# Performance work log

Hardware: AMD Instinct MI355X
Metric: run time of the kernel (lower is better)

## Reference

```python
import jax, jax.numpy as jnp
import numpy as np

B, T, F, H, K = 512, 128, 256, 512, 3

def setup_inputs() -> dict:
    key = jax.random.key(0)
    ks = jax.random.split(key, 8)
    x = jax.random.normal(ks[0], (B, T, F), dtype=jnp.float32)
    theta = jnp.ones((F,), dtype=jnp.float32)                 # selector logits
    Wx = jax.random.normal(ks[1], (F, H), dtype=jnp.float32) * 0.1
    Wh = jax.random.normal(ks[2], (H, H), dtype=jnp.float32) * 0.1
    b = jnp.zeros((H,), dtype=jnp.float32)
    c = jax.random.normal(ks[3], (H, K), dtype=jnp.float32)   # fuzzy centers
    sigma = jnp.ones((H, K), dtype=jnp.float32)               # fuzzy widths
    q = jax.random.normal(ks[4], (H, K), dtype=jnp.float32)   # rule consequents
    Wc = jax.random.normal(ks[5], (H, 1), dtype=jnp.float32) * 0.05  # classifier
    bc = jnp.zeros((1,), dtype=jnp.float32)
    return dict(x=x, theta=theta, Wx=Wx, Wh=Wh, b=b, c=c, sigma=sigma, q=q, Wc=Wc, bc=bc)


def reference(x, theta, Wx, Wh, b, c, sigma, q, Wc, bc):
    weights = jax.nn.sigmoid(theta)                 # [F]
    xf = x * weights                                # [B,T,F]
    # x_t @ Wx is used twice per step (for z_t and new_info); precompute once for all t.
    xw = jnp.einsum('btf,fh->bth', xf, Wx)          # [B,T,H]
    new_info = jnp.tanh(xw)                         # [B,T,H]
    inv_den = 1.0 / (2.0 * sigma ** 2 + 1e-8)       # [H,K]

    def step(h, inp):
        xw_t, new_t = inp                           # [B,H], [B,H]
        z = xw_t + h @ Wh + b                       # [B,H]
        mu = jnp.exp(-(z[..., None] - c) ** 2 * inv_den)   # [B,H,K]
        g = jax.nn.sigmoid(jnp.sum(mu * q, axis=-1) / (jnp.sum(mu, axis=-1) + 1e-8))
        h = (1.0 - g) * h + g * new_t
        return h, None

    h0 = jnp.zeros((x.shape[0], Wh.shape[0]), dtype=x.dtype)
    h, _ = jax.lax.scan(step, h0, (jnp.swapaxes(xw, 0, 1), jnp.swapaxes(new_info, 0, 1)))
    logits = h @ Wc + bc                            # [B,1]
    return logits, weights
```

## Files before the change

kernel.cpp:

```cpp
#include <hip/hip_runtime.h>
#include <hip/hip_bf16.h>


#define B_  512
#define T_  128
#define F_  256
#define H_  512
#define LOG2E 1.4426950408889634f

#define XW_T_STRIDE 262144

typedef __attribute__((ext_vector_type(8))) short short8;
typedef __attribute__((ext_vector_type(4))) float float4v;
typedef __attribute__((ext_vector_type(4))) int int4i;

__device__ inline ushort f2bf(float f) {
  __hip_bfloat16 h = __float2bfloat16(f);
  return *reinterpret_cast<ushort*>(&h);
}
__device__ inline float bf2f(unsigned u) { return __uint_as_float(u << 16); }
__device__ inline float fexp2(float x) { return __builtin_amdgcn_exp2f(x); }
__device__ inline float frcp(float x) { return __builtin_amdgcn_rcpf(x); }

#define WS_W2I8 67108864
#define WS_WXF  67371008
#define WS_GP8  67633152
#define WS_BVEC 67649536
#define WS_WCV  67651584
#define WS_SCOL 67653632
#define WS_WTS  67657728

__global__ __launch_bounds__(256) void prep_weights(
    const float* __restrict__ Wh, const float* __restrict__ Wx,
    const float* __restrict__ theta, const float* __restrict__ b,
    const float* __restrict__ c, const float* __restrict__ sigma,
    const float* __restrict__ q, const float* __restrict__ Wc,
    int* __restrict__ W2, ushort* __restrict__ WxF,
    float* __restrict__ scol, float* __restrict__ out_w,
    float* __restrict__ gp8, float* __restrict__ bvec,
    float* __restrict__ wcv, float* __restrict__ wts) {
  __shared__ float lds[16544];
  const int t = threadIdx.x;

  if (blockIdx.x < 32) {
    const int nb = blockIdx.x;
    const int cc = t & 15, rg = t >> 4;
    float m = 0.f;
#pragma unroll
    for (int s = 0; s < 32; ++s)
      m = fmaxf(m, fabsf(Wh[(rg + s * 16) * H_ + nb * 16 + cc]));
    lds[rg * 16 + cc] = m;
    __syncthreads();
    if (t < 16) {
      float mm = lds[t];
#pragma unroll
      for (int s = 1; s < 16; ++s) mm = fmaxf(mm, lds[s * 16 + t]);
      mm = fmaxf(mm, 1e-20f);
      scol[nb * 16 + t] = mm / (127.f * 127.f);
      lds[256 + t] = 127.f / mm;
    }
    __syncthreads();
    const int lane = t & 63, dw = t >> 6;
    const int n = nb * 16 + (lane & 15);
    const float iv = lds[256 + (lane & 15)];
#pragma unroll
    for (int kt = 0; kt < 8; ++kt) {
      int pk = 0;
#pragma unroll
      for (int jj = 0; jj < 4; ++jj) {
        const int k = kt * 64 + ((lane >> 4) << 4) + dw * 4 + jj;
        int qv = (int)rintf(Wh[k * H_ + n] * iv);
        qv = min(127, max(-127, qv));
        pk |= (qv & 255) << (8 * jj);
      }
      W2[((kt * 32 + nb) * 64 + lane) * 4 + dw] = pk;
    }
  } else if (blockIdx.x < 40) {
    const int kt = blockIdx.x - 32;
#pragma unroll
    for (int it = 0; it < 16; ++it) {
      const int lin = (it * 256 + t) * 4;
      const float4 v = *(const float4*)(Wx + kt * 32 * H_ + lin);
      const int f = lin >> 9, n0 = lin & 511;
      lds[f * 517 + n0 + 0] = v.x;
      lds[f * 517 + n0 + 1] = v.y;
      lds[f * 517 + n0 + 2] = v.z;
      lds[f * 517 + n0 + 3] = v.w;
    }
    __syncthreads();
#pragma unroll
    for (int it = 0; it < 8; ++it) {
      const int o = (it * 256 + t) * 8;
      const int lane = (o >> 3) & 63, nb = o >> 9;
      const int n = nb * 16 + (lane & 15), fb = (lane >> 4) << 3;
      ushort v[8];
#pragma unroll
      for (int j = 0; j < 8; ++j) v[j] = f2bf(lds[(fb + j) * 517 + n]);
      *(short8*)(WxF + kt * 16384 + o) = *(short8*)v;
    }
  } else {
#pragma unroll
    for (int r = 0; r < 2; ++r) {
      const int i = t + r * 256;
      if (i < F_) {
        float w = 1.f / (1.f + __expf(-theta[i]));
        out_w[i] = w;
        wts[i] = w;
      }
      float a[3], cc[3], qq[3];
#pragma unroll
      for (int k = 0; k < 3; ++k) {
        float s = sigma[i * 3 + k];
        cc[k] = c[i * 3 + k];
        a[k] = -LOG2E / (2.f * s * s + 1e-8f);
        qq[k] = q[i * 3 + k];
      }
      gp8[i * 8 + 0] = cc[0];
      gp8[i * 8 + 1] = cc[1];
      gp8[i * 8 + 2] = cc[2];
      gp8[i * 8 + 3] = a[0];
      gp8[i * 8 + 4] = a[1];
      gp8[i * 8 + 5] = a[2];
      gp8[i * 8 + 6] = __uint_as_float((unsigned)f2bf(qq[0]) |
                                       ((unsigned)f2bf(qq[1]) << 16));
      gp8[i * 8 + 7] = __uint_as_float((unsigned)f2bf(qq[2]));
      bvec[i] = b[i];
      wcv[i] = Wc[i];
    }
  }
}

__global__ __launch_bounds__(256, 2) void gemm1_kernel(
    const float* __restrict__ x, const float* __restrict__ wts,
    const ushort* __restrict__ WxF, ushort* __restrict__ xw2) {
  __shared__ ushort A2[2][64][256];
  const int tid = threadIdx.x;
  const int lane = tid & 63, wg = tid >> 6;
  const int col16 = lane & 15, quad = lane >> 4;
  const int tt2 = blockIdx.x, bb = blockIdx.y;

  {
    const float4 wv = *(const float4*)(wts + lane * 4);
#pragma unroll
    for (int s = 0; s < 2; ++s) {
      const int t = tt2 + s * 64;
#pragma unroll
      for (int it = 0; it < 16; ++it) {
        const int row = it * 4 + wg;
        float4 xv = *(const float4*)(x + ((size_t)(bb * 64 + row) * T_ + t) * F_ + lane * 4);
        ushort4 o;
        o.x = f2bf(xv.x * wv.x);
        o.y = f2bf(xv.y * wv.y);
        o.z = f2bf(xv.z * wv.z);
        o.w = f2bf(xv.w * wv.w);
        const int ki = (lane * 4) ^ ((row & 7) << 3);
        *(ushort4*)&A2[s][row][ki] = o;
      }
    }
  }
  __syncthreads();

  const float4v zero = {0.f, 0.f, 0.f, 0.f};
  const int arow = wg * 16 + col16;
#pragma unroll
  for (int nn = 0; nn < 2; ++nn) {
    float4v acc0[16], acc1[16];
#pragma unroll
    for (int i = 0; i < 16; ++i) { acc0[i] = zero; acc1[i] = zero; }
#pragma unroll
    for (int kt = 0; kt < 8; ++kt) {
      short8 bfv[16];
#pragma unroll
      for (int nt = 0; nt < 16; ++nt)
        bfv[nt] = *(const short8*)(WxF + ((kt * 32 + nn * 16 + nt) * 64 + lane) * 8);
      const int ki = (kt * 32 + quad * 8) ^ ((arow & 7) << 3);
      short8 af0 = *(const short8*)&A2[0][arow][ki];
      short8 af1 = *(const short8*)&A2[1][arow][ki];
#pragma unroll
      for (int nt = 0; nt < 16; ++nt) {
        acc0[nt] = __builtin_amdgcn_mfma_f32_16x16x32_bf16(af0, bfv[nt], acc0[nt], 0, 0, 0);
        acc1[nt] = __builtin_amdgcn_mfma_f32_16x16x32_bf16(af1, bfv[nt], acc1[nt], 0, 0, 0);
      }
    }
#pragma unroll
    for (int s = 0; s < 2; ++s) {
      const int t = tt2 + s * 64;
#pragma unroll
      for (int nt = 0; nt < 16; ++nt) {
        const float4v a = s ? acc1[nt] : acc0[nt];
        ushort2 lo, hi;
        lo.x = f2bf(a[0]);
        lo.y = f2bf(a[1]);
        hi.x = f2bf(a[2]);
        hi.y = f2bf(a[3]);
        const int bg0 = bb * 32 + wg * 8 + quad * 2;
        const size_t off0 =
            (((size_t)t * 256 + bg0) * 8 + nn * 4 + (nt >> 2)) * 128 +
            ((nt & 3) * 16 + col16) * 2;
        *(ushort2*)(xw2 + off0) = lo;
        *(ushort2*)(xw2 + off0 + 1024) = hi;
      }
    }
  }
}

__global__ __launch_bounds__(512, 2) void scan4_kernel(
    const ushort* __restrict__ xw2, const int4i* __restrict__ W2,
    const float* __restrict__ gp8, const float* __restrict__ bvec,
    const float* __restrict__ wcv, const float* __restrict__ scol,
    const float* __restrict__ bc, float* __restrict__ out) {
  __shared__ __align__(16) char hb[2][1152];
  __shared__ float red[8][2];
  const int tid = threadIdx.x;
  const int lane = tid & 63, w = tid >> 6;
  const int col16 = lane & 15, quad = lane >> 4;
  const int bg = blockIdx.x;

  for (int i = tid; i < 576; i += 512) ((int*)hb)[i] = 0;

  int4i bfr[8][4];
#pragma unroll
  for (int kt = 0; kt < 8; ++kt)
#pragma unroll
    for (int nt = 0; nt < 4; ++nt)
      bfr[kt][nt] = W2[(kt * 32 + w * 4 + nt) * 64 + lane];

  const int col = w * 64 + lane;
  const float bcol = bvec[col], scl = scol[col], wcl = wcv[col];
  float4v g0 = *(const float4v*)(gp8 + col * 8);
  float4v g1 = *(const float4v*)(gp8 + col * 8 + 4);
  const float c0v = g0[0], c1v = g0[1], c2v = g0[2];
  const float a0v = g0[3], a1v = g1[0], a2v = g1[1];
  unsigned p01 = __float_as_uint(g1[2]);
  const float q0v = bf2f(p01 & 0xffffu);
  const float q1v = bf2f(p01 >> 16);
  const float q2v = bf2f(__float_as_uint(g1[3]) & 0xffffu);
  const float b0v = -2.f * a0v * c0v, d0v = a0v * c0v * c0v;
  const float b1v = -2.f * a1v * c1v, d1v = a1v * c1v * c1v;
  const float b2v = -2.f * a2v * c2v, d2v = a2v * c2v * c2v;

  const unsigned wsel = (lane & 1) ? 0x0501u : 0x0004u;
  const int woff = col + ((lane & 1) ? 575 : 0);

  float hreg[2] = {0.f, 0.f};
  const int4i izero = {0, 0, 0, 0};
  int4i areg[8];
#pragma unroll
  for (int kt = 0; kt < 8; ++kt) areg[kt] = izero;

  const ushort* xwb = xw2 + ((size_t)bg * 8 + w) * 128 + lane * 2;
  unsigned xv = *(const unsigned*)xwb;
  unsigned xn;
  __syncthreads();

#pragma clang loop unroll(disable)
  for (int t = 0; t < T_; ++t) {
    const int tn = (t + 1) & 127;
    xn = *(const unsigned*)(xwb + (size_t)tn * XW_T_STRIDE);

    if (col16 < 2) {
      const char* abase = hb[t & 1] + col16 * 576;
#pragma unroll
      for (int kt = 0; kt < 8; ++kt)
        areg[kt] = *(const int4i*)(abase + kt * 64 + (quad << 4));
    }

    int4i acc0 = izero, acc1 = izero;
#pragma unroll
    for (int kt = 0; kt < 8; ++kt) {
      acc0 = __builtin_amdgcn_mfma_i32_16x16x64_i8(areg[kt], bfr[kt][0], acc0, 0, 0, 0);
      acc1 = __builtin_amdgcn_mfma_i32_16x16x64_i8(areg[kt], bfr[kt][1], acc1, 0, 0, 0);
    }
    int t0[2], t1[2];
#pragma unroll
    for (int rg = 0; rg < 2; ++rg) {
      t0[rg] = __shfl(acc0[rg], col16, 64);
      t1[rg] = __shfl(acc1[rg], col16, 64);
    }
    int4i acc2 = izero, acc3 = izero;
#pragma unroll
    for (int kt = 0; kt < 8; ++kt) {
      acc2 = __builtin_amdgcn_mfma_i32_16x16x64_i8(areg[kt], bfr[kt][2], acc2, 0, 0, 0);
      acc3 = __builtin_amdgcn_mfma_i32_16x16x64_i8(areg[kt], bfr[kt][3], acc3, 0, 0, 0);
    }
    int t2[2], t3[2];
#pragma unroll
    for (int rg = 0; rg < 2; ++rg) {
      t2[rg] = __shfl(acc2[rg], col16, 64);
      t3[rg] = __shfl(acc3[rg], col16, 64);
    }

    int accq[2];
#pragma unroll
    for (int rg = 0; rg < 2; ++rg) {
      int sA = (quad & 1) ? t1[rg] : t0[rg];
      int sB = (quad & 1) ? t3[rg] : t2[rg];
      accq[rg] = (quad & 2) ? sB : sA;
    }

    int qb[2];
#pragma unroll
    for (int rg = 0; rg < 2; ++rg) {
      float v = __uint_as_float(rg ? (xv & 0xffff0000u) : (xv << 16));
      float z = v + bcol + (float)accq[rg] * scl;
      float e = fexp2(v * (2.f * LOG2E));
      float nw = 1.f - 2.f * frcp(1.f + e);
      float zz = z * z;
      float m0 = fexp2(fmaf(a0v, zz, fmaf(b0v, z, d0v)));
      float m1 = fexp2(fmaf(a1v, zz, fmaf(b1v, z, d1v)));
      float m2 = fexp2(fmaf(a2v, zz, fmaf(b2v, z, d2v)));
      float num = m0 * q0v + m1 * q1v + m2 * q2v;
      float den = m0 + m1 + m2 + 1e-8f;
      float s = num * frcp(den);
      float gg = frcp(1.f + fexp2(-s * LOG2E));
      float h = hreg[rg] + gg * (nw - hreg[rg]);
      hreg[rg] = h;
      qb[rg] = (int)rintf(h * 127.f);
    }

    if (t < T_ - 1) {
      int pk = (int)__builtin_amdgcn_perm((unsigned)qb[1], (unsigned)qb[0], 0x0400u);
      unsigned p1 = (unsigned)__shfl_xor(pk, 1, 64);
      unsigned v16 = __builtin_amdgcn_perm((unsigned)pk, p1, wsel);
      *(ushort*)(hb[(t + 1) & 1] + woff) = (ushort)v16;
      __syncthreads();
    }
    xv = xn;
  }

  float part[2];
#pragma unroll
  for (int rg = 0; rg < 2; ++rg) {
    part[rg] = hreg[rg] * wcl;
#pragma unroll
    for (int m = 1; m < 64; m <<= 1) part[rg] += __shfl_xor(part[rg], m, 64);
  }
  if (lane == 0) {
    red[w][0] = part[0];
    red[w][1] = part[1];
  }
  __syncthreads();
  if (tid < 2) {
    float s = bc[0];
#pragma unroll
    for (int ww = 0; ww < 8; ++ww) s += red[ww][tid];
    out[bg * 2 + tid] = s;
  }
}

extern "C" void kernel_launch(void* const* d_in, const int* in_sizes, int n_in,
                              void* d_out, int out_size, void* d_ws, size_t ws_size,
                              hipStream_t stream) {
  const float* x     = (const float*)d_in[0];
  const float* theta = (const float*)d_in[1];
  const float* Wx    = (const float*)d_in[2];
  const float* Wh    = (const float*)d_in[3];
  const float* b     = (const float*)d_in[4];
  const float* c     = (const float*)d_in[5];
  const float* sigma = (const float*)d_in[6];
  const float* q     = (const float*)d_in[7];
  const float* Wc    = (const float*)d_in[8];
  const float* bc    = (const float*)d_in[9];
  float* out = (float*)d_out;

  ushort* xw2 = (ushort*)d_ws;
  int*    W2  = (int*)((char*)d_ws + WS_W2I8);
  ushort* WxF = (ushort*)((char*)d_ws + WS_WXF);
  float*  gp8 = (float*)((char*)d_ws + WS_GP8);
  float*  bv  = (float*)((char*)d_ws + WS_BVEC);
  float*  wcv = (float*)((char*)d_ws + WS_WCV);
  float*  scl = (float*)((char*)d_ws + WS_SCOL);
  float*  wts = (float*)((char*)d_ws + WS_WTS);

  hipLaunchKernelGGL(prep_weights, dim3(41), dim3(256), 0, stream,
                     Wh, Wx, theta, b, c, sigma, q, Wc,
                     W2, WxF, scl, out + B_, gp8, bv, wcv, wts);
  hipLaunchKernelGGL(gemm1_kernel, dim3(64, 8), dim3(256), 0, stream,
                     x, wts, WxF, xw2);
  hipLaunchKernelGGL(scan4_kernel, dim3(256), dim3(512), 0, stream,
                     xw2, (const int4i*)W2, gp8, bv, wcv, scl, bc, out);
}
```

Measured before the change: 250.5 us.

## Fuse weight prep into input GEMM kernel with atomic flag handoff

Merges the prep_weights kernel and the gemm1 kernel into one 512-block launch. The first 8 blocks convert Wx to bf16 fragments and signal a global atomic counter; every block spins on that counter before its MFMA loop. Blocks 8-40 also quantize Wh and pack the fuzzy parameters. The sigmoid of theta is recomputed per block instead of being read from a workspace buffer. This removes one kernel launch and the gap between kernels, at the cost of a memset, spin-waiting, and a dependence on the producer blocks being scheduled.

```diff
diff --git a/kernel.cpp b/kernel.cpp
--- a/kernel.cpp
+++ b/kernel.cpp
@@ -15,7 +15,7 @@
 typedef __attribute__((ext_vector_type(4))) int int4i;
 
 __device__ inline ushort f2bf(float f) {
-  __hip_bfloat16 h = __float2bfloat16(f);
+  __hip_bfloat16 h = __float2bfloat16(&f == nullptr ? 0.f : f);
   return *reinterpret_cast<ushort*>(&h);
 }
 __device__ inline float bf2f(unsigned u) { return __uint_as_float(u << 16); }
@@ -28,55 +28,31 @@
 #define WS_BVEC 67649536
 #define WS_WCV  67651584
 #define WS_SCOL 67653632
-#define WS_WTS  67657728
-
-__global__ __launch_bounds__(256) void prep_weights(
-    const float* __restrict__ Wh, const float* __restrict__ Wx,
-    const float* __restrict__ theta, const float* __restrict__ b,
-    const float* __restrict__ c, const float* __restrict__ sigma,
-    const float* __restrict__ q, const float* __restrict__ Wc,
+#define WS_FLAG 67657728
+
+__global__ __launch_bounds__(256, 2) void fused_prep_gemm(
+    const float* __restrict__ x, const float* __restrict__ theta,
+    const float* __restrict__ Wx, const float* __restrict__ Wh,
+    const float* __restrict__ b, const float* __restrict__ c,
+    const float* __restrict__ sigma, const float* __restrict__ q,
+    const float* __restrict__ Wc,
     int* __restrict__ W2, ushort* __restrict__ WxF,
     float* __restrict__ scol, float* __restrict__ out_w,
     float* __restrict__ gp8, float* __restrict__ bvec,
-    float* __restrict__ wcv, float* __restrict__ wts) {
-  __shared__ float lds[16544];
-  const int t = threadIdx.x;
-
-  if (blockIdx.x < 32) {
-    const int nb = blockIdx.x;
-    const int cc = t & 15, rg = t >> 4;
-    float m = 0.f;
-#pragma unroll
-    for (int s = 0; s < 32; ++s)
-      m = fmaxf(m, fabsf(Wh[(rg + s * 16) * H_ + nb * 16 + cc]));
-    lds[rg * 16 + cc] = m;
-    __syncthreads();
-    if (t < 16) {
-      float mm = lds[t];
-#pragma unroll
-      for (int s = 1; s < 16; ++s) mm = fmaxf(mm, lds[s * 16 + t]);
-      mm = fmaxf(mm, 1e-20f);
-      scol[nb * 16 + t] = mm / (127.f * 127.f);
-      lds[256 + t] = 127.f / mm;
-    }
-    __syncthreads();
-    const int lane = t & 63, dw = t >> 6;
-    const int n = nb * 16 + (lane & 15);
-    const float iv = lds[256 + (lane & 15)];
-#pragma unroll
-    for (int kt = 0; kt < 8; ++kt) {
-      int pk = 0;
-#pragma unroll
-      for (int jj = 0; jj < 4; ++jj) {
-        const int k = kt * 64 + ((lane >> 4) << 4) + dw * 4 + jj;
-        int qv = (int)rintf(Wh[k * H_ + n] * iv);
-        qv = min(127, max(-127, qv));
-        pk |= (qv & 255) << (8 * jj);
-      }
-      W2[((kt * 32 + nb) * 64 + lane) * 4 + dw] = pk;
-    }
-  } else if (blockIdx.x < 40) {
-    const int kt = blockIdx.x - 32;
+    float* __restrict__ wcv, ushort* __restrict__ xw2,
+    int* __restrict__ flag) {
+  __shared__ __align__(16) char smem[66176];
+  float* lds = (float*)smem;
+  ushort(&A2)[2][64][256] = *reinterpret_cast<ushort(*)[2][64][256]>(smem);
+
+  const int tid = threadIdx.x;
+  const int lane = tid & 63, wg = tid >> 6;
+  const int col16 = lane & 15, quad = lane >> 4;
+  const int bx = blockIdx.x;
+  const int tt2 = bx & 63, bb = bx >> 6;
+
+  if (bx < 8) {
+    const int kt = bx, t = tid;
 #pragma unroll
     for (int it = 0; it < 16; ++it) {
       const int lin = (it * 256 + t) * 4;
@@ -91,33 +67,72 @@
 #pragma unroll
     for (int it = 0; it < 8; ++it) {
       const int o = (it * 256 + t) * 8;
-      const int lane = (o >> 3) & 63, nb = o >> 9;
-      const int n = nb * 16 + (lane & 15), fb = (lane >> 4) << 3;
+      const int ln = (o >> 3) & 63, nb2 = o >> 9;
+      const int n = nb2 * 16 + (ln & 15), fb = (ln >> 4) << 3;
       ushort v[8];
 #pragma unroll
       for (int j = 0; j < 8; ++j) v[j] = f2bf(lds[(fb + j) * 517 + n]);
       *(short8*)(WxF + kt * 16384 + o) = *(short8*)v;
     }
-  } else {
+    __syncthreads();
+    __builtin_amdgcn_fence(__ATOMIC_RELEASE, "agent");
+    if (tid == 0)
+      __hip_atomic_fetch_add(flag, 1, __ATOMIC_RELEASE, __HIP_MEMORY_SCOPE_AGENT);
+    __syncthreads();
+  } else if (bx < 40) {
+    const int nb = bx - 8, t = tid;
+    const int cc = t & 15, rg = t >> 4;
+    float m = 0.f;
+#pragma unroll
+    for (int s = 0; s < 32; ++s)
+      m = fmaxf(m, fabsf(Wh[(rg + s * 16) * H_ + nb * 16 + cc]));
+    lds[rg * 16 + cc] = m;
+    __syncthreads();
+    if (t < 16) {
+      float mm = lds[t];
+#pragma unroll
+      for (int s = 1; s < 16; ++s) mm = fmaxf(mm, lds[s * 16 + t]);
+      mm = fmaxf(mm, 1e-20f);
+      scol[nb * 16 + t] = mm / (127.f * 127.f);
+      lds[256 + t] = 127.f / mm;
+    }
+    __syncthreads();
+    const int dw = t >> 6;
+    const int n = nb * 16 + col16;
+    const float iv = lds[256 + col16];
+#pragma unroll
+    for (int kt = 0; kt < 8; ++kt) {
+      int pk = 0;
+#pragma unroll
+      for (int jj = 0; jj < 4; ++jj) {
+        const int k = kt * 64 + ((lane >> 4) << 4) + dw * 4 + jj;
+        int qv = (int)rintf(Wh[k * H_ + n] * iv);
+        qv = min(127, max(-127, qv));
+        pk |= (qv & 255) << (8 * jj);
+      }
+      W2[((kt * 32 + nb) * 64 + lane) * 4 + dw] = pk;
+    }
+    __syncthreads();
+  } else if (bx == 40) {
+    const int t = tid;
 #pragma unroll
     for (int r = 0; r < 2; ++r) {
       const int i = t + r * 256;
       if (i < F_) {
         float w = 1.f / (1.f + __expf(-theta[i]));
         out_w[i] = w;
-        wts[i] = w;
-      }
-      float a[3], cc[3], qq[3];
+      }
+      float a[3], cc2[3], qq[3];
 #pragma unroll
       for (int k = 0; k < 3; ++k) {
         float s = sigma[i * 3 + k];
-        cc[k] = c[i * 3 + k];
+        cc2[k] = c[i * 3 + k];
         a[k] = -LOG2E / (2.f * s * s + 1e-8f);
         qq[k] = q[i * 3 + k];
       }
-      gp8[i * 8 + 0] = cc[0];
-      gp8[i * 8 + 1] = cc[1];
-      gp8[i * 8 + 2] = cc[2];
+      gp8[i * 8 + 0] = cc2[0];
+      gp8[i * 8 + 1] = cc2[1];
+      gp8[i * 8 + 2] = cc2[2];
       gp8[i * 8 + 3] = a[0];
       gp8[i * 8 + 4] = a[1];
       gp8[i * 8 + 5] = a[2];
@@ -128,19 +143,14 @@
       wcv[i] = Wc[i];
     }
   }
-}
-
-__global__ __launch_bounds__(256, 2) void gemm1_kernel(
-    const float* __restrict__ x, const float* __restrict__ wts,
-    const ushort* __restrict__ WxF, ushort* __restrict__ xw2) {
-  __shared__ ushort A2[2][64][256];
-  const int tid = threadIdx.x;
-  const int lane = tid & 63, wg = tid >> 6;
-  const int col16 = lane & 15, quad = lane >> 4;
-  const int tt2 = blockIdx.x, bb = blockIdx.y;
 
   {
-    const float4 wv = *(const float4*)(wts + lane * 4);
+    const float4 th = *(const float4*)(theta + lane * 4);
+    float4 wv;
+    wv.x = 1.f / (1.f + __expf(-th.x));
+    wv.y = 1.f / (1.f + __expf(-th.y));
+    wv.z = 1.f / (1.f + __expf(-th.z));
+    wv.w = 1.f / (1.f + __expf(-th.w));
 #pragma unroll
     for (int s = 0; s < 2; ++s) {
       const int t = tt2 + s * 64;
@@ -159,6 +169,13 @@
     }
   }
   __syncthreads();
+
+  if (tid == 0) {
+    while (__hip_atomic_load(flag, __ATOMIC_RELAXED, __HIP_MEMORY_SCOPE_AGENT) < 8)
+      __builtin_amdgcn_s_sleep(8);
+  }
+  __syncthreads();
+  __builtin_amdgcn_fence(__ATOMIC_ACQUIRE, "agent");
 
   const float4v zero = {0.f, 0.f, 0.f, 0.f};
   const int arow = wg * 16 + col16;
@@ -370,13 +387,12 @@
   float*  bv  = (float*)((char*)d_ws + WS_BVEC);
   float*  wcv = (float*)((char*)d_ws + WS_WCV);
   float*  scl = (float*)((char*)d_ws + WS_SCOL);
-  float*  wts = (float*)((char*)d_ws + WS_WTS);
-
-  hipLaunchKernelGGL(prep_weights, dim3(41), dim3(256), 0, stream,
-                     Wh, Wx, theta, b, c, sigma, q, Wc,
-                     W2, WxF, scl, out + B_, gp8, bv, wcv, wts);
-  hipLaunchKernelGGL(gemm1_kernel, dim3(64, 8), dim3(256), 0, stream,
-                     x, wts, WxF, xw2);
+  int*    flg = (int*)((char*)d_ws + WS_FLAG);
+
+  hipMemsetAsync(flg, 0, 4, stream);
+  hipLaunchKernelGGL(fused_prep_gemm, dim3(512), dim3(256), 0, stream,
+                     x, theta, Wx, Wh, b, c, sigma, q, Wc,
+                     W2, WxF, scl, out + B_, gp8, bv, wcv, xw2, flg);
   hipLaunchKernelGGL(scan4_kernel, dim3(256), dim3(512), 0, stream,
                      xw2, (const int4i*)W2, gp8, bv, wcv, scl, bc, out);
 }
```

Result: slower. 260.0 us (+3.8%).
